# Kernel tuning notes

Hardware: AMD Instinct MI355X
Metric: run time of the kernel (lower is better)

Reference implementation:

```python
import jax, jax.numpy as jnp
import numpy as np

N_NODES = 50000
N_EDGES = 1600000
IN_FEAT = 256
HIDDEN = 128
N_CLASSES = 16


def gcn_conv(x, edge_index, W, b, n_nodes):
    """PyG GCNConv: x' = D^{-1/2} (A+I) D^{-1/2} (x @ W) + b."""
    h = x @ W  # project first (PyG order), messages are in out_dim
    src, dst = edge_index[0], edge_index[1]
    loops = jnp.arange(n_nodes, dtype=src.dtype)
    src = jnp.concatenate([src, loops])
    dst = jnp.concatenate([dst, loops])
    # degree of A+I (count incoming edges incl. self loop)
    deg = jax.ops.segment_sum(jnp.ones_like(dst, dtype=h.dtype), dst, num_segments=n_nodes)
    dis = jax.lax.rsqrt(deg)  # deg >= 1 thanks to self loops
    norm = dis[src] * dis[dst]  # [E+N]
    msgs = h[src] * norm[:, None]  # gather + scale
    out = jax.ops.segment_sum(msgs, dst, num_segments=n_nodes)  # scatter-add
    return out + b


def setup_inputs() -> dict:
    key = jax.random.key(0)
    k_x, k_e, k_w1, k_b1, k_w2, k_b2 = jax.random.split(key, 6)
    x = jax.random.normal(k_x, (N_NODES, IN_FEAT), dtype=jnp.float32)
    edge_index = jax.random.randint(k_e, (2, N_EDGES), 0, N_NODES, dtype=jnp.int64)
    s1 = 1.0 / np.sqrt(IN_FEAT)
    s2 = 1.0 / np.sqrt(HIDDEN)
    W1 = jax.random.uniform(k_w1, (IN_FEAT, HIDDEN), jnp.float32, -s1, s1)
    b1 = jax.random.uniform(k_b1, (HIDDEN,), jnp.float32, -s1, s1)
    W2 = jax.random.uniform(k_w2, (HIDDEN, N_CLASSES), jnp.float32, -s2, s2)
    b2 = jax.random.uniform(k_b2, (N_CLASSES,), jnp.float32, -s2, s2)
    return {"x": x, "edge_index": edge_index, "W1": W1, "b1": b1, "W2": W2, "b2": b2}


def reference(x, edge_index, W1, b1, W2, b2):
    n = x.shape[0]
    h = gcn_conv(x, edge_index, W1, b1, n)
    h = jax.nn.relu(h)
    logits = gcn_conv(h, edge_index, W2, b2, n)
    return logits, jax.nn.softmax(logits, axis=1)
```

## Files before the change

### kernel.cpp

```cpp
#include <hip/hip_runtime.h>
#include <hip/hip_bf16.h>
#include <math.h>

#define N_NODES 50000
#define N_EDGES 1600000
#define IN_FEAT 256
#define HIDDEN 128
#define N_CLASSES 16

#define ECHUNK 2048
#define NCHK 782
#define NBKT 196
#define BCAP 10240
#define CSTR 16

typedef __attribute__((ext_vector_type(8))) short short8;
typedef __attribute__((ext_vector_type(4))) float floatx4;

__device__ __forceinline__ unsigned short f2bf(float f) {
    unsigned u = __float_as_uint(f);
    return (unsigned short)((u + 0x7fffu + ((u >> 16) & 1u)) >> 16);
}

__device__ __forceinline__ unsigned pk2bf(float a, float b) {
    __hip_bfloat162 h = __float22bfloat162_rn(make_float2(a, b));
    union { __hip_bfloat162 h; unsigned u; } cv;
    cv.h = h;
    return cv.u;
}

__device__ __forceinline__ float bflo(unsigned u) { return __uint_as_float(u << 16); }
__device__ __forceinline__ float bfhi(unsigned u) { return __uint_as_float(u & 0xffff0000u); }

__global__ __launch_bounds__(256) void scatter_edges2(const int* __restrict__ src,
                                                      const int* __restrict__ dst,
                                                      int* __restrict__ cursor,
                                                      unsigned int* __restrict__ sorted,
                                                      const float* __restrict__ W1,
                                                      unsigned short* __restrict__ w1t) {
    __shared__ int hloc[256];
    int t = threadIdx.x;
    hloc[t] = 0;
    if (blockIdx.x < HIDDEN)
        w1t[blockIdx.x * IN_FEAT + t] = f2bf(W1[t * HIDDEN + blockIdx.x]);
    __syncthreads();
    int base = blockIdx.x * ECHUNK;
    int end = min(base + ECHUNK, N_EDGES);
    for (int i = base + t; i < end; i += 256)
        atomicAdd(&hloc[dst[i] >> 8], 1);
    __syncthreads();
    int cnt = hloc[t];
    int lbase = 0;
    if (cnt > 0) lbase = t * BCAP + atomicAdd(&cursor[t * CSTR], cnt);
    __syncthreads();
    hloc[t] = lbase;
    __syncthreads();
    for (int i = base + t; i < end; i += 256) {
        int d = dst[i];
        int s = src[i];
        int pos = atomicAdd(&hloc[d >> 8], 1);
        sorted[pos] = ((unsigned)d << 16) | (unsigned)s;
    }
}

__global__ __launch_bounds__(512) void build_csr2(const unsigned int* __restrict__ sorted,
                                                  const int* __restrict__ cursor,
                                                  int* __restrict__ rs,
                                                  int* __restrict__ re,
                                                  float* __restrict__ dis,
                                                  unsigned short* __restrict__ csr_src) {
    __shared__ int cnt[256];
    __shared__ int roff[256];
    int t = threadIdx.x;
    int bkt = blockIdx.x;
    int ebase = bkt * BCAP;
    int eend = ebase + cursor[bkt * CSTR];
    if (t < 256) cnt[t] = 0;
    __syncthreads();
    for (int i = ebase + t; i < eend; i += 512)
        atomicAdd(&cnt[(sorted[i] >> 16) & 255], 1);
    __syncthreads();
    int v = 0;
    if (t < 256) { v = cnt[t]; roff[t] = v; }
    __syncthreads();
    for (int off = 1; off < 256; off <<= 1) {
        int x = (t < 256 && t >= off) ? roff[t - off] : 0;
        __syncthreads();
        if (t < 256) roff[t] += x;
        __syncthreads();
    }
    if (t < 256) {
        int excl = roff[t] - v;
        int node = bkt * 256 + t;
        if (node < N_NODES) {
            rs[node] = ebase + excl;
            re[node] = ebase + excl + v;
            dis[node] = 1.0f / sqrtf((float)(v + 1));
        }
        cnt[t] = ebase + excl;
    }
    __syncthreads();
    for (int i = ebase + t; i < eend; i += 512) {
        unsigned e = sorted[i];
        int pos = atomicAdd(&cnt[(e >> 16) & 255], 1);
        csr_src[pos] = (unsigned short)(e & 0xffffu);
    }
}

#define XCHDW 260
#define KBLK (4 * XCHDW)

__global__ __launch_bounds__(256) void gemm1_mfma(const float* __restrict__ x,
                                                  const unsigned short* __restrict__ w1t,
                                                  const float* __restrict__ dis,
                                                  unsigned int* __restrict__ g1) {
    __shared__ float xs[8 * KBLK];
    int tid = threadIdx.x;
    int w = tid >> 6;
    int lane = tid & 63;
    int quad = lane >> 4;
    int c = lane & 15;
    int row_base = blockIdx.x * 32;
    int col_base = w * 32;

    int st_row = min(row_base + 8 * w + (lane >> 3), N_NODES - 1);
    const float* gp1 = x + (size_t)st_row * IN_FEAT + (lane & 7) * 4;
#pragma unroll
    for (int kk = 0; kk < 8; ++kk)
        __builtin_amdgcn_global_load_lds(
            (const __attribute__((address_space(1))) void*)(gp1 + kk * 32),
            (__attribute__((address_space(3))) void*)&xs[kk * KBLK + w * XCHDW], 16, 0, 0);

    floatx4 acc[2][2] = {};
    const unsigned short* bp[2];
#pragma unroll
    for (int nt = 0; nt < 2; ++nt)
        bp[nt] = w1t + (size_t)(col_base + nt * 16 + c) * IN_FEAT + quad * 8;

    int dwoff[2];
#pragma unroll
    for (int rt = 0; rt < 2; ++rt) {
        int rit = rt * 16 + c;
        dwoff[rt] = (rit >> 3) * XCHDW + (rit & 7) * 32 + quad * 8;
    }

    __syncthreads();

#pragma unroll
    for (int kk = 0; kk < 8; ++kk) {
        short8 b[2];
#pragma unroll
        for (int nt = 0; nt < 2; ++nt)
            b[nt] = *(const short8*)(bp[nt] + kk * 32);
        short8 a[2];
#pragma unroll
        for (int rt = 0; rt < 2; ++rt) {
            float4 f0 = *(const float4*)&xs[kk * KBLK + dwoff[rt]];
            float4 f1 = *(const float4*)&xs[kk * KBLK + dwoff[rt] + 4];
            union { short8 s; unsigned u[4]; } au;
            au.u[0] = pk2bf(f0.x, f0.y);
            au.u[1] = pk2bf(f0.z, f0.w);
            au.u[2] = pk2bf(f1.x, f1.y);
            au.u[3] = pk2bf(f1.z, f1.w);
            a[rt] = au.s;
        }
#pragma unroll
        for (int rt = 0; rt < 2; ++rt)
#pragma unroll
            for (int nt = 0; nt < 2; ++nt)
                acc[rt][nt] = __builtin_amdgcn_mfma_f32_16x16x32_bf16(a[rt], b[nt], acc[rt][nt], 0, 0, 0);
    }

    bool evenlane = (lane & 1) == 0;
#pragma unroll
    for (int rt = 0; rt < 2; ++rt) {
#pragma unroll
        for (int reg = 0; reg < 4; ++reg) {
            int row = row_base + rt * 16 + quad * 4 + reg;
            float dv = dis[min(row, N_NODES - 1)];
#pragma unroll
            for (int nt = 0; nt < 2; ++nt) {
                float v = acc[rt][nt][reg] * dv;
                float vo = __shfl_xor(v, 1);
                if (evenlane && row < N_NODES) {
                    unsigned pkd = (unsigned)f2bf(v) | ((unsigned)f2bf(vo) << 16);
                    int col = col_base + nt * 16 + c;
                    g1[(size_t)(col >> 5) * (N_NODES * 16) + (size_t)row * 16 + ((col & 31) >> 1)] = pkd;
                }
            }
        }
    }
}

__global__ __launch_bounds__(256) void agg1_sliced(const uint4* __restrict__ g1,
                                                   const int* __restrict__ rs,
                                                   const int* __restrict__ re,
                                                   const unsigned short* __restrict__ csr_src,
                                                   const float* __restrict__ dis,
                                                   const float* __restrict__ b1,
                                                   const float* __restrict__ W2,
                                                   float* __restrict__ g2p,
                                                   int bi0) {
    __shared__ float w2s[32 * 16];
    __shared__ float rbuf[4][16][36];
    int tid = threadIdx.x;
    int bi = blockIdx.x + bi0;
    int bucket = bi >> 4;
    int xcd = bi & 7;
    int slice = xcd >> 1;
    int quarter = ((bi >> 3) & 1) * 2 + (xcd & 1);

    for (int i = tid; i < 512; i += 256) w2s[i] = W2[slice * 512 + i];
    __syncthreads();

    int wave = tid >> 6, lane = tid & 63;
    int g = lane >> 2, m4 = lane & 3;
    const uint4* plane = g1 + (size_t)slice * (N_NODES * 4);
    float* gp = g2p + (size_t)slice * ((size_t)N_NODES * 16);
    int node = bucket * 256 + quarter * 64 + wave * 16 + g;
    bool alive = (node < N_NODES);

#define ACC8(u) do { a0 += bflo((u).x); a1 += bfhi((u).x); a2 += bflo((u).y); a3 += bfhi((u).y); \
                     a4 += bflo((u).z); a5 += bfhi((u).z); a6 += bflo((u).w); a7 += bfhi((u).w); } while (0)
#define GATH(IV, U0, U1, U2, U3) do {                       \
        int j0_ = (int)((IV).x & 0xffffu);                  \
        int j1_ = (int)((IV).x >> 16);                      \
        int j2_ = (int)((IV).y & 0xffffu);                  \
        int j3_ = (int)((IV).y >> 16);                      \
        U0 = plane[(size_t)j0_ * 4 + m4];                   \
        U1 = plane[(size_t)j1_ * 4 + m4];                   \
        U2 = plane[(size_t)j2_ * 4 + m4];                   \
        U3 = plane[(size_t)j3_ * 4 + m4];                   \
    } while (0)

    if (alive) {
        uint4 su = plane[(size_t)node * 4 + m4];
        float a0 = bflo(su.x), a1 = bfhi(su.x), a2 = bflo(su.y), a3 = bfhi(su.y);
        float a4 = bflo(su.z), a5 = bfhi(su.z), a6 = bflo(su.w), a7 = bfhi(su.w);
        int e = rs[node], e1v = re[node];
        while ((e & 3) && e < e1v) {
            int j = csr_src[e];
            uint4 u = plane[(size_t)j * 4 + m4];
            ACC8(u);
            ++e;
        }
        int nb = (e1v - e) >> 2;
        if (nb >= 2) {
            uint2 Ia = *(const uint2*)&csr_src[e];
            uint2 Ib = *(const uint2*)&csr_src[e + 4];
            uint4 A0, A1, A2, A3, B0, B1, B2, B3;
            GATH(Ia, A0, A1, A2, A3);
            GATH(Ib, B0, B1, B2, B3);
            __builtin_amdgcn_sched_barrier(0);
            int b = 2;
            while (b + 2 <= nb) {
                Ia = *(const uint2*)&csr_src[e + 4 * b];
                ACC8(A0); ACC8(A1); ACC8(A2); ACC8(A3);
                GATH(Ia, A0, A1, A2, A3);
                __builtin_amdgcn_sched_barrier(0);
                Ib = *(const uint2*)&csr_src[e + 4 * b + 4];
                ACC8(B0); ACC8(B1); ACC8(B2); ACC8(B3);
                GATH(Ib, B0, B1, B2, B3);
                __builtin_amdgcn_sched_barrier(0);
                b += 2;
            }
            int rem = nb - b;
            ACC8(A0); ACC8(A1); ACC8(A2); ACC8(A3);
            if (rem) {
                Ia = *(const uint2*)&csr_src[e + 4 * b];
                GATH(Ia, A0, A1, A2, A3);
            }
            ACC8(B0); ACC8(B1); ACC8(B2); ACC8(B3);
            if (rem) { ACC8(A0); ACC8(A1); ACC8(A2); ACC8(A3); }
            e += 4 * nb;
        } else if (nb >= 1) {
            uint2 Iv = *(const uint2*)&csr_src[e];
            uint4 U0, U1, U2, U3;
            GATH(Iv, U0, U1, U2, U3);
            ACC8(U0); ACC8(U1); ACC8(U2); ACC8(U3);
            e += 4;
        }
        while (e < e1v) {
            int j = csr_src[e];
            uint4 u = plane[(size_t)j * 4 + m4];
            ACC8(u);
            ++e;
        }

        float dv = dis[node];
        float4 bb0 = *(const float4*)&b1[slice * 32 + 8 * m4];
        float4 bb1 = *(const float4*)&b1[slice * 32 + 8 * m4 + 4];
        float4 r0, r1;
        r0.x = fmaxf(fmaf(dv, a0, bb0.x), 0.f);
        r0.y = fmaxf(fmaf(dv, a1, bb0.y), 0.f);
        r0.z = fmaxf(fmaf(dv, a2, bb0.z), 0.f);
        r0.w = fmaxf(fmaf(dv, a3, bb0.w), 0.f);
        r1.x = fmaxf(fmaf(dv, a4, bb1.x), 0.f);
        r1.y = fmaxf(fmaf(dv, a5, bb1.y), 0.f);
        r1.z = fmaxf(fmaf(dv, a6, bb1.z), 0.f);
        r1.w = fmaxf(fmaf(dv, a7, bb1.w), 0.f);
        *(float4*)&rbuf[wave][g][8 * m4] = r0;
        *(float4*)&rbuf[wave][g][8 * m4 + 4] = r1;
    }
    __builtin_amdgcn_sched_barrier(0);
    if (alive) {
        float p0 = 0.f, p1 = 0.f, p2 = 0.f, p3 = 0.f;
#pragma unroll
        for (int fb = 0; fb < 8; ++fb) {
            float4 rv = *(const float4*)&rbuf[wave][g][fb * 4];
            float4 w0 = *(const float4*)&w2s[(fb * 4 + 0) * 16 + 4 * m4];
            float4 w1 = *(const float4*)&w2s[(fb * 4 + 1) * 16 + 4 * m4];
            float4 w2 = *(const float4*)&w2s[(fb * 4 + 2) * 16 + 4 * m4];
            float4 w3 = *(const float4*)&w2s[(fb * 4 + 3) * 16 + 4 * m4];
            p0 = fmaf(rv.x, w0.x, p0); p1 = fmaf(rv.x, w0.y, p1);
            p2 = fmaf(rv.x, w0.z, p2); p3 = fmaf(rv.x, w0.w, p3);
            p0 = fmaf(rv.y, w1.x, p0); p1 = fmaf(rv.y, w1.y, p1);
            p2 = fmaf(rv.y, w1.z, p2); p3 = fmaf(rv.y, w1.w, p3);
            p0 = fmaf(rv.z, w2.x, p0); p1 = fmaf(rv.z, w2.y, p1);
            p2 = fmaf(rv.z, w2.z, p2); p3 = fmaf(rv.z, w2.w, p3);
            p0 = fmaf(rv.w, w3.x, p0); p1 = fmaf(rv.w, w3.y, p1);
            p2 = fmaf(rv.w, w3.z, p2); p3 = fmaf(rv.w, w3.w, p3);
        }
        float4 pv; pv.x = p0; pv.y = p1; pv.z = p2; pv.w = p3;
        *(float4*)&gp[(size_t)node * 16 + 4 * m4] = pv;
    }
#undef GATH
#undef ACC8
}

__global__ __launch_bounds__(256) void g2_reduce(float* __restrict__ g2p,
                                                 const float* __restrict__ dis) {
    int i = blockIdx.x * 256 + threadIdx.x;
    if (i >= N_NODES * 4) return;
    const size_t PS = (size_t)N_NODES * 16 / 4;
    const float4* p = (const float4*)g2p;
    float4 a = p[i];
    float4 b = p[i + PS];
    float4 c = p[i + 2 * PS];
    float4 d = p[i + 3 * PS];
    float dv = dis[i >> 2];
    float4 r;
    r.x = dv * ((a.x + b.x) + (c.x + d.x));
    r.y = dv * ((a.y + b.y) + (c.y + d.y));
    r.z = dv * ((a.z + b.z) + (c.z + d.z));
    r.w = dv * ((a.w + b.w) + (c.w + d.w));
    ((float4*)g2p)[i] = r;
}

__global__ __launch_bounds__(256) void agg2_softmax(const float4* __restrict__ g2,
                                                    const int* __restrict__ rs,
                                                    const int* __restrict__ re,
                                                    const unsigned short* __restrict__ csr_src,
                                                    const float* __restrict__ dis,
                                                    const float* __restrict__ b2,
                                                    float* __restrict__ out) {
    int tid = threadIdx.x;
    int wave = tid >> 6, lane = tid & 63;
    int g = lane >> 2, m4 = lane & 3;
    int node = blockIdx.x * 64 + wave * 16 + g;
    if (node >= N_NODES) return;

    float4 acc = g2[(size_t)node * 4 + m4];

#define ACC4(u) do { acc.x += (u).x; acc.y += (u).y; acc.z += (u).z; acc.w += (u).w; } while (0)
#define GATH4(IV, U0, U1, U2, U3) do {                      \
        int j0_ = (int)((IV).x & 0xffffu);                  \
        int j1_ = (int)((IV).x >> 16);                      \
        int j2_ = (int)((IV).y & 0xffffu);                  \
        int j3_ = (int)((IV).y >> 16);                      \
        U0 = g2[(size_t)j0_ * 4 + m4];                      \
        U1 = g2[(size_t)j1_ * 4 + m4];                      \
        U2 = g2[(size_t)j2_ * 4 + m4];                      \
        U3 = g2[(size_t)j3_ * 4 + m4];                      \
    } while (0)

    int e = rs[node], e1v = re[node];
    while ((e & 3) && e < e1v) {
        int j = csr_src[e];
        float4 u = g2[(size_t)j * 4 + m4];
        ACC4(u);
        ++e;
    }
    int nb = (e1v - e) >> 2;
    if (nb >= 2) {
        uint2 Ia = *(const uint2*)&csr_src[e];
        uint2 Ib = *(const uint2*)&csr_src[e + 4];
        float4 A0, A1, A2, A3, B0, B1, B2, B3;
        GATH4(Ia, A0, A1, A2, A3);
        GATH4(Ib, B0, B1, B2, B3);
        __builtin_amdgcn_sched_barrier(0);
        int b = 2;
        while (b + 2 <= nb) {
            Ia = *(const uint2*)&csr_src[e + 4 * b];
            ACC4(A0); ACC4(A1); ACC4(A2); ACC4(A3);
            GATH4(Ia, A0, A1, A2, A3);
            __builtin_amdgcn_sched_barrier(0);
            Ib = *(const uint2*)&csr_src[e + 4 * b + 4];
            ACC4(B0); ACC4(B1); ACC4(B2); ACC4(B3);
            GATH4(Ib, B0, B1, B2, B3);
            __builtin_amdgcn_sched_barrier(0);
            b += 2;
        }
        int rem = nb - b;
        ACC4(A0); ACC4(A1); ACC4(A2); ACC4(A3);
        if (rem) {
            Ia = *(const uint2*)&csr_src[e + 4 * b];
            GATH4(Ia, A0, A1, A2, A3);
        }
        ACC4(B0); ACC4(B1); ACC4(B2); ACC4(B3);
        if (rem) { ACC4(A0); ACC4(A1); ACC4(A2); ACC4(A3); }
        e += 4 * nb;
    } else if (nb >= 1) {
        uint2 Iv = *(const uint2*)&csr_src[e];
        float4 U0, U1, U2, U3;
        GATH4(Iv, U0, U1, U2, U3);
        ACC4(U0); ACC4(U1); ACC4(U2); ACC4(U3);
        e += 4;
    }
    while (e < e1v) {
        int j = csr_src[e];
        float4 u = g2[(size_t)j * 4 + m4];
        ACC4(u);
        ++e;
    }
#undef GATH4
#undef ACC4

    float dv = dis[node];
    float4 bb = *(const float4*)&b2[4 * m4];
    float4 lg;
    lg.x = fmaf(dv, acc.x, bb.x);
    lg.y = fmaf(dv, acc.y, bb.y);
    lg.z = fmaf(dv, acc.z, bb.z);
    lg.w = fmaf(dv, acc.w, bb.w);
    ((float4*)out)[(size_t)node * 4 + m4] = lg;

    float m = fmaxf(fmaxf(lg.x, lg.y), fmaxf(lg.z, lg.w));
    m = fmaxf(m, __shfl_xor(m, 1));
    m = fmaxf(m, __shfl_xor(m, 2));
    float4 ex;
    ex.x = expf(lg.x - m); ex.y = expf(lg.y - m);
    ex.z = expf(lg.z - m); ex.w = expf(lg.w - m);
    float s = (ex.x + ex.y) + (ex.z + ex.w);
    s += __shfl_xor(s, 1);
    s += __shfl_xor(s, 2);
    float inv = 1.0f / s;
    ex.x *= inv; ex.y *= inv; ex.z *= inv; ex.w *= inv;
    ((float4*)out)[(size_t)N_NODES * 4 + (size_t)node * 4 + m4] = ex;
}


extern "C" void kernel_launch(void* const* d_in, const int* in_sizes, int n_in,
                              void* d_out, int out_size, void* d_ws, size_t ws_size,
                              hipStream_t stream) {
    const float* x  = (const float*)d_in[0];
    const int*   ei = (const int*)d_in[1];
    const float* W1 = (const float*)d_in[2];
    const float* b1 = (const float*)d_in[3];
    const float* W2 = (const float*)d_in[4];
    const float* b2 = (const float*)d_in[5];
    float* out = (float*)d_out;

    char* ws = (char*)d_ws;
    size_t off = 0;
    auto alloc = [&](size_t bytes) -> char* {
        char* p = ws + off;
        off = (off + bytes + 511) & ~(size_t)511;
        return p;
    };
    int*   cursor   = (int*)alloc(256 * CSTR * 4);
    float* dis      = (float*)alloc(N_NODES * 4);
    int*   rs       = (int*)alloc(N_NODES * 4);
    int*   re       = (int*)alloc(N_NODES * 4);
    unsigned short* w1t = (unsigned short*)alloc((size_t)HIDDEN * IN_FEAT * 2);
    unsigned short* csr_src = (unsigned short*)alloc((size_t)NBKT * BCAP * 2);
    unsigned int* g1 = (unsigned int*)alloc((size_t)N_NODES * 64 * 4);
    float* g2p      = (float*)alloc(4 * (size_t)N_NODES * N_CLASSES * 4);
    unsigned int* sorted = (unsigned int*)g1;
    (void)ws_size; (void)in_sizes; (void)n_in; (void)out_size;

    const int* src = ei;
    const int* dst = ei + N_EDGES;

    hipMemsetAsync(cursor, 0, 256 * CSTR * 4, stream);
    scatter_edges2<<<NCHK, 256, 0, stream>>>(src, dst, cursor, sorted, W1, w1t);
    build_csr2<<<NBKT, 512, 0, stream>>>(sorted, cursor, rs, re, dis, csr_src);

    gemm1_mfma<<<(N_NODES + 31) / 32, 256, 0, stream>>>(x, w1t, dis, g1);
    agg1_sliced<<<NBKT * 8, 256, 0, stream>>>((const uint4*)g1, rs, re, csr_src, dis, b1, W2, g2p, 0);
    agg1_sliced<<<NBKT * 8, 256, 0, stream>>>((const uint4*)g1, rs, re, csr_src, dis, b1, W2, g2p, NBKT * 8);
    g2_reduce<<<(N_NODES * 4 + 255) / 256, 256, 0, stream>>>(g2p, dis);
    agg2_softmax<<<N_NODES / 64 + 1, 256, 0, stream>>>((const float4*)g2p, rs, re, csr_src, dis, b2, out);
}
```

Before: 230.2 us.

## Split hidden features into two 64-wide slices instead of four 32-wide

Changes the g1 layout from four 32-column bf16 planes to two 64-column planes. Each node's gather now reads a 128-byte row per edge using 8 lanes, and the two agg1 launches are merged into one launch covering both slices. The partial buffer for layer 2 shrinks to two slices, so g2_reduce sums fewer partials. This halves the number of times each CSR edge list is walked, in exchange for fewer nodes per wave and a per-lane layer-2 product computed with scalar shared-memory reads.

```diff
diff --git a/kernel.cpp b/kernel.cpp
--- a/kernel.cpp
+++ b/kernel.cpp
@@ -185,7 +185,7 @@
                 if (evenlane && row < N_NODES) {
                     unsigned pkd = (unsigned)f2bf(v) | ((unsigned)f2bf(vo) << 16);
                     int col = col_base + nt * 16 + c;
-                    g1[(size_t)(col >> 5) * (N_NODES * 16) + (size_t)row * 16 + ((col & 31) >> 1)] = pkd;
+                    g1[(size_t)(col >> 6) * ((size_t)N_NODES * 32) + (size_t)row * 32 + ((col & 63) >> 1)] = pkd;
                 }
             }
         }
@@ -199,25 +199,24 @@
                                                    const float* __restrict__ dis,
                                                    const float* __restrict__ b1,
                                                    const float* __restrict__ W2,
-                                                   float* __restrict__ g2p,
-                                                   int bi0) {
-    __shared__ float w2s[32 * 16];
-    __shared__ float rbuf[4][16][36];
+                                                   float* __restrict__ g2p) {
+    __shared__ float w2s[64 * 16];
+    __shared__ float rbuf[4][8][68];
     int tid = threadIdx.x;
-    int bi = blockIdx.x + bi0;
+    int bi = blockIdx.x;
     int bucket = bi >> 4;
     int xcd = bi & 7;
-    int slice = xcd >> 1;
-    int quarter = ((bi >> 3) & 1) * 2 + (xcd & 1);
-
-    for (int i = tid; i < 512; i += 256) w2s[i] = W2[slice * 512 + i];
+    int slice = xcd >> 2;
+    int sub = ((bi >> 3) & 1) * 4 + (xcd & 3);
+
+    for (int i = tid; i < 1024; i += 256) w2s[i] = W2[slice * 1024 + i];
     __syncthreads();
 
     int wave = tid >> 6, lane = tid & 63;
-    int g = lane >> 2, m4 = lane & 3;
-    const uint4* plane = g1 + (size_t)slice * (N_NODES * 4);
+    int g = lane >> 3, m = lane & 7;
+    const uint4* plane = g1 + (size_t)slice * ((size_t)N_NODES * 8);
     float* gp = g2p + (size_t)slice * ((size_t)N_NODES * 16);
-    int node = bucket * 256 + quarter * 64 + wave * 16 + g;
+    int node = bucket * 256 + sub * 32 + wave * 8 + g;
     bool alive = (node < N_NODES);
 
 #define ACC8(u) do { a0 += bflo((u).x); a1 += bfhi((u).x); a2 += bflo((u).y); a3 += bfhi((u).y); \
@@ -227,20 +226,20 @@
         int j1_ = (int)((IV).x >> 16);                      \
         int j2_ = (int)((IV).y & 0xffffu);                  \
         int j3_ = (int)((IV).y >> 16);                      \
-        U0 = plane[(size_t)j0_ * 4 + m4];                   \
-        U1 = plane[(size_t)j1_ * 4 + m4];                   \
-        U2 = plane[(size_t)j2_ * 4 + m4];                   \
-        U3 = plane[(size_t)j3_ * 4 + m4];                   \
+        U0 = plane[(size_t)j0_ * 8 + m];                    \
+        U1 = plane[(size_t)j1_ * 8 + m];                    \
+        U2 = plane[(size_t)j2_ * 8 + m];                    \
+        U3 = plane[(size_t)j3_ * 8 + m];                    \
     } while (0)
 
     if (alive) {
-        uint4 su = plane[(size_t)node * 4 + m4];
+        uint4 su = plane[(size_t)node * 8 + m];
         float a0 = bflo(su.x), a1 = bfhi(su.x), a2 = bflo(su.y), a3 = bfhi(su.y);
         float a4 = bflo(su.z), a5 = bfhi(su.z), a6 = bflo(su.w), a7 = bfhi(su.w);
         int e = rs[node], e1v = re[node];
         while ((e & 3) && e < e1v) {
             int j = csr_src[e];
-            uint4 u = plane[(size_t)j * 4 + m4];
+            uint4 u = plane[(size_t)j * 8 + m];
             ACC8(u);
             ++e;
         }
@@ -282,14 +281,14 @@
         }
         while (e < e1v) {
             int j = csr_src[e];
-            uint4 u = plane[(size_t)j * 4 + m4];
+            uint4 u = plane[(size_t)j * 8 + m];
             ACC8(u);
             ++e;
         }
 
         float dv = dis[node];
-        float4 bb0 = *(const float4*)&b1[slice * 32 + 8 * m4];
-        float4 bb1 = *(const float4*)&b1[slice * 32 + 8 * m4 + 4];
+        float4 bb0 = *(const float4*)&b1[slice * 64 + 8 * m];
+        float4 bb1 = *(const float4*)&b1[slice * 64 + 8 * m + 4];
         float4 r0, r1;
         r0.x = fmaxf(fmaf(dv, a0, bb0.x), 0.f);
         r0.y = fmaxf(fmaf(dv, a1, bb0.y), 0.f);
@@ -299,30 +298,25 @@
         r1.y = fmaxf(fmaf(dv, a5, bb1.y), 0.f);
         r1.z = fmaxf(fmaf(dv, a6, bb1.z), 0.f);
         r1.w = fmaxf(fmaf(dv, a7, bb1.w), 0.f);
-        *(float4*)&rbuf[wave][g][8 * m4] = r0;
-        *(float4*)&rbuf[wave][g][8 * m4 + 4] = r1;
+        *(float4*)&rbuf[wave][g][8 * m] = r0;
+        *(float4*)&rbuf[wave][g][8 * m + 4] = r1;
     }
     __builtin_amdgcn_sched_barrier(0);
     if (alive) {
-        float p0 = 0.f, p1 = 0.f, p2 = 0.f, p3 = 0.f;
-#pragma unroll
-        for (int fb = 0; fb < 8; ++fb) {
+        float p0 = 0.f, p1 = 0.f;
+#pragma unroll
+        for (int fb = 0; fb < 16; ++fb) {
             float4 rv = *(const float4*)&rbuf[wave][g][fb * 4];
-            float4 w0 = *(const float4*)&w2s[(fb * 4 + 0) * 16 + 4 * m4];
-            float4 w1 = *(const float4*)&w2s[(fb * 4 + 1) * 16 + 4 * m4];
-            float4 w2 = *(const float4*)&w2s[(fb * 4 + 2) * 16 + 4 * m4];
-            float4 w3 = *(const float4*)&w2s[(fb * 4 + 3) * 16 + 4 * m4];
-            p0 = fmaf(rv.x, w0.x, p0); p1 = fmaf(rv.x, w0.y, p1);
-            p2 = fmaf(rv.x, w0.z, p2); p3 = fmaf(rv.x, w0.w, p3);
-            p0 = fmaf(rv.y, w1.x, p0); p1 = fmaf(rv.y, w1.y, p1);
-            p2 = fmaf(rv.y, w1.z, p2); p3 = fmaf(rv.y, w1.w, p3);
-            p0 = fmaf(rv.z, w2.x, p0); p1 = fmaf(rv.z, w2.y, p1);
-            p2 = fmaf(rv.z, w2.z, p2); p3 = fmaf(rv.z, w2.w, p3);
-            p0 = fmaf(rv.w, w3.x, p0); p1 = fmaf(rv.w, w3.y, p1);
-            p2 = fmaf(rv.w, w3.z, p2); p3 = fmaf(rv.w, w3.w, p3);
-        }
-        float4 pv; pv.x = p0; pv.y = p1; pv.z = p2; pv.w = p3;
-        *(float4*)&gp[(size_t)node * 16 + 4 * m4] = pv;
+            p0 = fmaf(rv.x, w2s[(fb * 4 + 0) * 16 + 2 * m], p0);
+            p1 = fmaf(rv.x, w2s[(fb * 4 + 0) * 16 + 2 * m + 1], p1);
+            p0 = fmaf(rv.y, w2s[(fb * 4 + 1) * 16 + 2 * m], p0);
+            p1 = fmaf(rv.y, w2s[(fb * 4 + 1) * 16 + 2 * m + 1], p1);
+            p0 = fmaf(rv.z, w2s[(fb * 4 + 2) * 16 + 2 * m], p0);
+            p1 = fmaf(rv.z, w2s[(fb * 4 + 2) * 16 + 2 * m + 1], p1);
+            p0 = fmaf(rv.w, w2s[(fb * 4 + 3) * 16 + 2 * m], p0);
+            p1 = fmaf(rv.w, w2s[(fb * 4 + 3) * 16 + 2 * m + 1], p1);
+        }
+        *(float2*)&gp[(size_t)node * 16 + 2 * m] = make_float2(p0, p1);
     }
 #undef GATH
 #undef ACC8
@@ -336,14 +330,12 @@
     const float4* p = (const float4*)g2p;
     float4 a = p[i];
     float4 b = p[i + PS];
-    float4 c = p[i + 2 * PS];
-    float4 d = p[i + 3 * PS];
     float dv = dis[i >> 2];
     float4 r;
-    r.x = dv * ((a.x + b.x) + (c.x + d.x));
-    r.y = dv * ((a.y + b.y) + (c.y + d.y));
-    r.z = dv * ((a.z + b.z) + (c.z + d.z));
-    r.w = dv * ((a.w + b.w) + (c.w + d.w));
+    r.x = dv * (a.x + b.x);
+    r.y = dv * (a.y + b.y);
+    r.z = dv * (a.z + b.z);
+    r.w = dv * (a.w + b.w);
     ((float4*)g2p)[i] = r;
 }
 
@@ -475,7 +467,7 @@
     unsigned short* w1t = (unsigned short*)alloc((size_t)HIDDEN * IN_FEAT * 2);
     unsigned short* csr_src = (unsigned short*)alloc((size_t)NBKT * BCAP * 2);
     unsigned int* g1 = (unsigned int*)alloc((size_t)N_NODES * 64 * 4);
-    float* g2p      = (float*)alloc(4 * (size_t)N_NODES * N_CLASSES * 4);
+    float* g2p      = (float*)alloc(2 * (size_t)N_NODES * N_CLASSES * 4);
     unsigned int* sorted = (unsigned int*)g1;
     (void)ws_size; (void)in_sizes; (void)n_in; (void)out_size;
 
@@ -487,8 +479,7 @@
     build_csr2<<<NBKT, 512, 0, stream>>>(sorted, cursor, rs, re, dis, csr_src);
 
     gemm1_mfma<<<(N_NODES + 31) / 32, 256, 0, stream>>>(x, w1t, dis, g1);
-    agg1_sliced<<<NBKT * 8, 256, 0, stream>>>((const uint4*)g1, rs, re, csr_src, dis, b1, W2, g2p, 0);
-    agg1_sliced<<<NBKT * 8, 256, 0, stream>>>((const uint4*)g1, rs, re, csr_src, dis, b1, W2, g2p, NBKT * 8);
+    agg1_sliced<<<NBKT * 16, 256, 0, stream>>>((const uint4*)g1, rs, re, csr_src, dis, b1, W2, g2p);
     g2_reduce<<<(N_NODES * 4 + 255) / 256, 256, 0, stream>>>(g2p, dis);
     agg2_softmax<<<N_NODES / 64 + 1, 256, 0, stream>>>((const float4*)g2p, rs, re, csr_src, dis, b2, out);
 }
```

Result: faster. 223.4 us (-3.0%).
